# Performance work log

Measured on AMD Instinct MI355X. Metric: run time of the kernel, lower is better.

The kernel has to match this reference:

```python
import jax, jax.numpy as jnp
import numpy as np

H, W, D = 56, 56, 28            # input_resolution
WS = (7, 7, 7)                  # window size (Wh, Ww, Wd)
SS = (3, 3, 3)                  # shift size
DIM = 96
NH = 3
HD = DIM // NH
N = WS[0] * WS[1] * WS[2]       # 343 tokens per window
NW = (H // WS[0]) * (W // WS[1]) * (D // WS[2])  # 256 windows


def _rel_pos_index():
    Wd, Wh, Ww = WS
    coords = np.stack(np.meshgrid(np.arange(Wd), np.arange(Wh), np.arange(Ww), indexing='ij'))
    cf = coords.reshape(3, -1)
    rel = (cf[:, :, None] - cf[:, None, :]).transpose(1, 2, 0)
    rel[:, :, 0] += Wd - 1
    rel[:, :, 1] += Wh - 1
    rel[:, :, 2] += Ww - 1
    rel[:, :, 0] *= (2 * Wh - 1) * (2 * Ww - 1)
    rel[:, :, 1] *= (2 * Ww - 1)
    return rel.sum(-1)  # (N, N)


def _attn_mask():
    img = np.zeros((H, W, D), np.float32)
    def slices(w, s):
        return (slice(0, -w), slice(-w, -s), slice(-s, None))
    cnt = 0
    for hs in slices(WS[0], SS[0]):
        for ws in slices(WS[1], SS[1]):
            for ds in slices(WS[2], SS[2]):
                img[hs, ws, ds] = cnt
                cnt += 1
    mw = img.reshape(H // WS[0], WS[0], W // WS[1], WS[1], D // WS[2], WS[2])
    mw = mw.transpose(0, 2, 4, 1, 3, 5).reshape(-1, N)  # (NW, N)
    am = mw[:, None, :] - mw[:, :, None]
    return np.where(am != 0, np.float32(-100.0), np.float32(0.0))


REL_IDX = jnp.asarray(_rel_pos_index())
ATTN_MASK = jnp.asarray(_attn_mask())  # (NW, N, N)


def _ln(x, g, b, eps=1e-5):
    m = x.mean(-1, keepdims=True)
    v = jnp.mean((x - m) ** 2, -1, keepdims=True)
    return (x - m) * jax.lax.rsqrt(v + eps) * g + b


def _forward(x, n1g, n1b, qkv_w, qkv_b, rpb, proj_w, proj_b,
             n2g, n2b, fc1_w, fc1_b, fc2_w, fc2_b):
    B, L, C = x.shape
    shortcut = x
    h = _ln(x, n1g, n1b).reshape(B, H, W, D, C)
    # cyclic shift
    h = jnp.roll(h, (-SS[0], -SS[1], -SS[2]), axis=(1, 2, 3))
    # window partition -> (B*NW, N, C)
    h = h.reshape(B, H // WS[0], WS[0], W // WS[1], WS[1], D // WS[2], WS[2], C)
    h = h.transpose(0, 1, 3, 5, 2, 4, 6, 7).reshape(-1, N, C)
    # qkv
    qkv = (h @ qkv_w + qkv_b).reshape(-1, N, 3, NH, HD).transpose(2, 0, 3, 1, 4)
    q, k, v = qkv[0] * (HD ** -0.5), qkv[1], qkv[2]  # (B*NW, NH, N, HD)
    attn = jnp.einsum('bhnd,bhmd->bhnm', q, k)
    bias = rpb[REL_IDX.reshape(-1)].reshape(N, N, NH).transpose(2, 0, 1)
    attn = attn + bias[None]
    # shifted-window mask
    attn = attn.reshape(B, NW, NH, N, N) + ATTN_MASK[None, :, None]
    attn = jax.nn.softmax(attn.reshape(-1, NH, N, N), axis=-1)
    o = jnp.einsum('bhnm,bhmd->bhnd', attn, v).transpose(0, 2, 1, 3).reshape(-1, N, C)
    o = o @ proj_w + proj_b
    # window reverse
    o = o.reshape(B, H // WS[0], W // WS[1], D // WS[2], WS[0], WS[1], WS[2], C)
    o = o.transpose(0, 1, 4, 2, 5, 3, 6, 7).reshape(B, H, W, D, C)
    o = jnp.roll(o, SS, axis=(1, 2, 3)).reshape(B, L, C)
    x = shortcut + o
    h2 = _ln(x, n2g, n2b)
    h2 = jax.nn.gelu(h2 @ fc1_w + fc1_b, approximate=False) @ fc2_w + fc2_b
    return x + h2


def setup_inputs() -> dict:
    key = jax.random.key(0)
    ks = jax.random.split(key, 6)
    C, FF = DIM, 4 * DIM
    f32 = jnp.float32
    return {
        'x': jax.random.normal(ks[0], (1, H * W * D, C), f32),
        'n1g': jnp.ones((C,), f32), 'n1b': jnp.zeros((C,), f32),
        'qkv_w': jax.random.normal(ks[1], (C, 3 * C), f32) * 0.02,
        'qkv_b': jnp.zeros((3 * C,), f32),
        'rpb': jax.random.normal(ks[2], ((2 * WS[0] - 1) * (2 * WS[1] - 1) * (2 * WS[2] - 1), NH), f32) * 0.02,
        'proj_w': jax.random.normal(ks[3], (C, C), f32) * 0.02,
        'proj_b': jnp.zeros((C,), f32),
        'n2g': jnp.ones((C,), f32), 'n2b': jnp.zeros((C,), f32),
        'fc1_w': jax.random.normal(ks[4], (C, FF), f32) * 0.02,
        'fc1_b': jnp.zeros((FF,), f32),
        'fc2_w': jax.random.normal(ks[5], (FF, C), f32) * 0.02,
        'fc2_b': jnp.zeros((C,), f32),
    }


def reference(x, n1g, n1b, qkv_w, qkv_b, rpb, proj_w, proj_b,
              n2g, n2b, fc1_w, fc1_b, fc2_w, fc2_b):
    return _forward(x, n1g, n1b, qkv_w, qkv_b, rpb, proj_w, proj_b,
                    n2g, n2b, fc1_w, fc1_b, fc2_w, fc2_b)
```

## Files before the change

kernel.cpp:

```cpp
#include <hip/hip_runtime.h>
#include <hip/hip_bf16.h>


#define L_TOK 87808

typedef unsigned int uint;
typedef __attribute__((ext_vector_type(8))) short short8;
typedef __attribute__((ext_vector_type(4))) float f32x4;

__device__ __forceinline__ float bflo(uint u){ union{uint x; float f;} a; a.x = u << 16; return a.f; }
__device__ __forceinline__ float bfhi(uint u){ union{uint x; float f;} a; a.x = u & 0xffff0000u; return a.f; }
__device__ __forceinline__ float bfval(unsigned short w){ union{uint x; float f;} a; a.x = (uint)w << 16; return a.f; }
__device__ __forceinline__ unsigned short f2bfbits(float f){
  union{float f; uint u;} a; a.f = f;
  uint u = a.u;
  u += 0x7fffu + ((u >> 16) & 1u);
  return (unsigned short)(u >> 16);
}
__device__ __forceinline__ unsigned short bfb(float f){
  __hip_bfloat16 h = __float2bfloat16(f);
  return *reinterpret_cast<unsigned short*>(&h);
}
__device__ __forceinline__ uint pkbf(float a, float b){
  return ((uint)bfb(b) << 16) | (uint)bfb(a);
}
__device__ __forceinline__ uint pack2(float a, float b){
  return ((uint)f2bfbits(b) << 16) | (uint)f2bfbits(a);
}
__device__ __forceinline__ uint4 pack8(const float* p){
  uint4 u;
  u.x = pack2(p[0], p[1]); u.y = pack2(p[2], p[3]);
  u.z = pack2(p[4], p[5]); u.w = pack2(p[6], p[7]);
  return u;
}
__device__ __forceinline__ uint4 pack8g(const float* gp){
  float t[8];
  *(float4*)&t[0] = *(const float4*)gp;
  *(float4*)&t[4] = *(const float4*)(gp + 4);
  return pack8(t);
}
__device__ __forceinline__ float gelu_f(float v){
  const float ax = fabsf(v) * 0.70710678118654752f;
  const float t  = 1.0f / (1.0f + 0.3275911f * ax);
  const float poly = t*(0.254829592f + t*(-0.284496736f + t*(1.421413741f +
                     t*(-1.453152027f + t*1.061405429f))));
  float erfv = 1.0f - poly * __expf(-ax*ax);
  erfv = copysignf(erfv, v);
  return 0.5f * v * (1.0f + erfv);
}
__device__ __forceinline__ uint gt_of_row(uint row){
  const uint win = row / 343u, n = row % 343u;
  const uint wh = win >> 5, ww = (win >> 2) & 7u, wd = win & 3u;
  const uint ih = n / 49u, rr = n % 49u, iw = rr / 7u, id = rr % 7u;
  uint gh = wh*7u + ih + 3u; if (gh >= 56u) gh -= 56u;
  uint gw = ww*7u + iw + 3u; if (gw >= 56u) gw -= 56u;
  uint gd = wd*7u + id + 3u; if (gd >= 28u) gd -= 28u;
  return ((gh*56u + gw)*28u + gd) * 96u;
}

__global__ __launch_bounds__(256)
void k_tr(const float* __restrict__ src, unsigned short* __restrict__ dst,
          int K, int N)
{
  const int idx = blockIdx.x * 256 + threadIdx.x;
  if (idx < K * N) {
    const int n = idx / K, k = idx % K;
    dst[idx] = f2bfbits(src[(size_t)k * N + n]);
  }
}

__global__ __launch_bounds__(256)
void k_tr4(const float* __restrict__ qkvw, unsigned short* __restrict__ qkvwt,
           const float* __restrict__ pw,   unsigned short* __restrict__ pwt,
           const float* __restrict__ f1w,  unsigned short* __restrict__ w1t,
           const float* __restrict__ f2w,  unsigned short* __restrict__ w2t)
{
  const int b = blockIdx.x, tid = threadIdx.x;
  const float* src; unsigned short* dst; int K, N, idx;
  if (b < 108)      { src = qkvw; dst = qkvwt; K = 96;  N = 288; idx = b*256 + tid; }
  else if (b < 144) { src = pw;   dst = pwt;   K = 96;  N = 96;  idx = (b-108)*256 + tid; }
  else if (b < 288) { src = f1w;  dst = w1t;   K = 96;  N = 384; idx = (b-144)*256 + tid; }
  else              { src = f2w;  dst = w2t;   K = 384; N = 96;  idx = (b-288)*256 + tid; }
  if (idx < K * N) {
    const int n = idx / K, k = idx % K;
    dst[idx] = f2bfbits(src[(size_t)k * N + n]);
  }
}

__global__ __launch_bounds__(256)
void k_mb(const float* __restrict__ rpbg, unsigned short* __restrict__ MB)
{
  const int idx = blockIdx.x * 256 + threadIdx.x;
  const int cls = idx / (3*352*352);
  const int rem = idx - cls * (3*352*352);
  const int h = rem / (352*352);
  const int rem2 = rem - h * (352*352);
  const int q = rem2 / 352;
  const int k = rem2 - q * 352;
  unsigned short v = 0xFF80;
  if (q < 343 && k < 343) {
    const int q0 = q/49, q1 = (q%49)/7, q2 = q%7;
    const int k0 = k/49, k1 = (k%49)/7, k2 = k%7;
    const int bq = q0*169 + q1*13 + q2;
    const int bk = k0*169 + k1*13 + k2;
    float bias = rpbg[(size_t)(bq - bk + 1098)*3 + h];
    int cq = 0, ck = 0;
    if (cls & 4) { cq += ((q0 < 4) ? 1 : 2)*9; ck += ((k0 < 4) ? 1 : 2)*9; }
    if (cls & 2) { cq += ((q1 < 4) ? 1 : 2)*3; ck += ((k1 < 4) ? 1 : 2)*3; }
    if (cls & 1) { cq += (q2 < 4) ? 1 : 2;     ck += (k2 < 4) ? 1 : 2; }
    if (cq != ck) bias -= 100.0f;
    v = f2bfbits(bias);
  }
  MB[idx] = v;
}

__global__ __launch_bounds__(256)
void k_qkv_ln(const float* __restrict__ x,
              const float* __restrict__ n1g,
              const float* __restrict__ n1b,
              const unsigned short* __restrict__ qkvwt,
              const float* __restrict__ bias, size_t headStride,
              __hip_bfloat16* __restrict__ qb,
              __hip_bfloat16* __restrict__ kb,
              __hip_bfloat16* __restrict__ vb)
{
  __shared__ __align__(16) unsigned short As[64][104];
  __shared__ uint srcOff[64];
  __shared__ float gLds[96], bLds[96];
  __shared__ float pSum[256], pSq[256];
  __shared__ float mLds[64], sLds[64];

  const int tid = threadIdx.x;
  const int wave = tid >> 6, lane = tid & 63;
  const int row0 = blockIdx.x * 64;

  if (tid < 64) srcOff[tid] = gt_of_row((uint)(row0 + tid));
  if (tid < 96) { gLds[tid] = n1g[tid]; bLds[tid] = n1b[tid]; }
  __syncthreads();

  for (int i = tid; i < 768; i += 256) {
    const int r = i / 12, kk = (i % 12) * 8;
    *(uint4*)&As[r][kk] = pack8g(x + srcOff[r] + kk);
  }
  __syncthreads();

  {
    const int r = tid & 63, seg = tid >> 6;
    float s = 0.0f, sq = 0.0f;
    #pragma unroll
    for (int j3 = 0; j3 < 3; ++j3) {
      const uint4 u = *(const uint4*)&As[r][seg*24 + j3*8];
      float v[8];
      v[0]=bflo(u.x); v[1]=bfhi(u.x); v[2]=bflo(u.y); v[3]=bfhi(u.y);
      v[4]=bflo(u.z); v[5]=bfhi(u.z); v[6]=bflo(u.w); v[7]=bfhi(u.w);
      #pragma unroll
      for (int j = 0; j < 8; ++j) { s += v[j]; sq += v[j]*v[j]; }
    }
    pSum[tid] = s; pSq[tid] = sq;
  }
  __syncthreads();
  if (tid < 64) {
    const float s  = pSum[tid] + pSum[tid+64] + pSum[tid+128] + pSum[tid+192];
    const float sq = pSq[tid] + pSq[tid+64] + pSq[tid+128] + pSq[tid+192];
    const float mean = s * (1.0f/96.0f);
    mLds[tid] = mean;
    sLds[tid] = rsqrtf(sq*(1.0f/96.0f) - mean*mean + 1e-5f);
  }
  __syncthreads();
  for (int i = tid; i < 768; i += 256) {
    const int r = i / 12, kk = (i % 12) * 8;
    uint4 u = *(uint4*)&As[r][kk];
    const float m = mLds[r], sc = sLds[r];
    float v[8];
    v[0]=bflo(u.x); v[1]=bfhi(u.x); v[2]=bflo(u.y); v[3]=bfhi(u.y);
    v[4]=bflo(u.z); v[5]=bfhi(u.z); v[6]=bflo(u.w); v[7]=bfhi(u.w);
    #pragma unroll
    for (int j = 0; j < 8; ++j) v[j] = (v[j] - m)*sc*gLds[kk+j] + bLds[kk+j];
    *(uint4*)&As[r][kk] = pack8(v);
  }
  __syncthreads();

  f32x4 acc[18];
  #pragma unroll
  for (int i = 0; i < 18; ++i) acc[i] = (f32x4){0.f, 0.f, 0.f, 0.f};
  const int ml = lane & 15, q8 = (lane >> 4) * 8;
  #pragma unroll
  for (int kc = 0; kc < 3; ++kc) {
    const short8 a = *(const short8*)&As[wave*16 + ml][kc*32 + q8];
    #pragma unroll
    for (int nt = 0; nt < 18; ++nt) {
      const short8 b = *(const short8*)(qkvwt + (size_t)(nt*16 + ml)*96 + kc*32 + q8);
      acc[nt] = __builtin_amdgcn_mfma_f32_16x16x32_bf16(a, b, acc[nt], 0, 0, 0);
    }
  }

  const float qscale = 0.17677669529663687f;
  #pragma unroll
  for (int nt = 0; nt < 18; ++nt) {
    const int nbase = nt * 16;
    const int part = nbase / 96;
    const int rem  = nbase - part * 96;
    const int h    = rem >> 5;
    const int dbase= rem & 31;
    __hip_bfloat16* base = (part == 0) ? qb : ((part == 1) ? kb : vb);
    __hip_bfloat16* dst = base + (size_t)h * headStride;
    const float bv = bias[nbase + ml];
    #pragma unroll
    for (int r = 0; r < 4; ++r) {
      const size_t row = (size_t)(row0 + wave*16 + (lane >> 4)*4 + r);
      float v = acc[nt][r] + bv;
      if (part == 0) v *= qscale;
      dst[row*32 + dbase + ml] = __float2bfloat16(v);
    }
  }
}

template<bool BF16OUT>
__global__ __launch_bounds__(256, 4)
void k_attn_v10(const __hip_bfloat16* __restrict__ qg,
                const __hip_bfloat16* __restrict__ kg,
                const __hip_bfloat16* __restrict__ vg,
                size_t headStride,
                const unsigned short* __restrict__ MB,
                void* __restrict__ obp)
{
  __shared__ __align__(16) unsigned short vt[32*344 + 16];
  __shared__ __align__(16) unsigned short Pc[4][16*56];
  __shared__ float lred[4][16];

  const int tid = threadIdx.x;
  const int wave = tid >> 6, lane = tid & 63;
  const uint win = blockIdx.x;
  const int hh = (int)blockIdx.y;
  const int mtBase = (int)blockIdx.z * 11;
  const size_t wbase = (size_t)hh * headStride + (size_t)win * (343*32);
  const unsigned short* qw = (const unsigned short*)qg + wbase;
  const unsigned short* kw = (const unsigned short*)kg + wbase;
  const unsigned short* vw = (const unsigned short*)vg + wbase;

  const uint wh = win >> 5, ww = (win >> 2) & 7u, wd = win & 3u;
  const int cls = ((wh == 7u) ? 4 : 0) | ((ww == 7u) ? 2 : 0) | ((wd == 3u) ? 1 : 0);
  const unsigned short* MBh = MB + ((size_t)cls*3 + hh) * (352*352);

  for (int t = tid; t < 343; t += 256) {
    const uint4* src = (const uint4*)(vw + (size_t)t*32);
    #pragma unroll
    for (int c4 = 0; c4 < 4; ++c4) {
      const uint4 u = src[c4];
      const int d = c4*8;
      vt[(d+0)*344 + t] = (unsigned short)(u.x & 0xffffu);
      vt[(d+1)*344 + t] = (unsigned short)(u.x >> 16);
      vt[(d+2)*344 + t] = (unsigned short)(u.y & 0xffffu);
      vt[(d+3)*344 + t] = (unsigned short)(u.y >> 16);
      vt[(d+4)*344 + t] = (unsigned short)(u.z & 0xffffu);
      vt[(d+5)*344 + t] = (unsigned short)(u.z >> 16);
      vt[(d+6)*344 + t] = (unsigned short)(u.w & 0xffffu);
      vt[(d+7)*344 + t] = (unsigned short)(u.w >> 16);
    }
  }
  if (tid < 32) vt[tid*344 + 343] = 0;
  if (tid < 16) vt[32*344 + tid] = 0;
  __syncthreads();

  const int ml = lane & 15, g = lane >> 4, g8 = g*8;
  unsigned short* Pw = &Pc[wave][0];

  for (int mt = mtBase + wave; mt < mtBase + 11; mt += 4) {
    const int q = mt*16 + ml;
    const short8 qf = *(const short8*)(qw + (size_t)q*32 + g8);
    const unsigned short* MBq = MBh + (size_t)q * 352;
    float l = 0.0f;
    f32x4 o0 = {0.f,0.f,0.f,0.f}, o1 = {0.f,0.f,0.f,0.f};

    for (int kc = 0; kc < 11; ++kc) {
      const short8 kf0 = *(const short8*)(kw + (size_t)(kc*32 + ml)*32 + g8);
      const short8 kf1 = *(const short8*)(kw + (size_t)(kc*32 + 16 + ml)*32 + g8);
      f32x4 s0 = __builtin_amdgcn_mfma_f32_16x16x32_bf16(kf0, qf, (f32x4){0.f,0.f,0.f,0.f}, 0, 0, 0);
      f32x4 s1 = __builtin_amdgcn_mfma_f32_16x16x32_bf16(kf1, qf, (f32x4){0.f,0.f,0.f,0.f}, 0, 0, 0);

      const ushort4 u0 = *(const ushort4*)(MBq + kc*32 + 4*g);
      const ushort4 u1 = *(const ushort4*)(MBq + kc*32 + 16 + 4*g);

      float p0 = __expf(s0[0] + bfval(u0.x));
      float p1 = __expf(s0[1] + bfval(u0.y));
      float p2 = __expf(s0[2] + bfval(u0.z));
      float p3 = __expf(s0[3] + bfval(u0.w));
      float p4 = __expf(s1[0] + bfval(u1.x));
      float p5 = __expf(s1[1] + bfval(u1.y));
      float p6 = __expf(s1[2] + bfval(u1.z));
      float p7 = __expf(s1[3] + bfval(u1.w));
      l += ((p0 + p1) + (p2 + p3)) + ((p4 + p5) + (p6 + p7));

      uint2 wlo, whi;
      wlo.x = pkbf(p0, p1); wlo.y = pkbf(p2, p3);
      whi.x = pkbf(p4, p5); whi.y = pkbf(p6, p7);
      *(uint2*)&Pw[ml*56 + 4*g]      = wlo;
      *(uint2*)&Pw[ml*56 + 16 + 4*g] = whi;

      const short8 pf  = *(const short8*)&Pw[ml*56 + g8];
      const short8 vf0 = *(const short8*)&vt[(size_t)ml*344 + kc*32 + g8];
      const short8 vf1 = *(const short8*)&vt[(size_t)(16 + ml)*344 + kc*32 + g8];
      o0 = __builtin_amdgcn_mfma_f32_16x16x32_bf16(pf, vf0, o0, 0, 0, 0);
      o1 = __builtin_amdgcn_mfma_f32_16x16x32_bf16(pf, vf1, o1, 0, 0, 0);
    }

    l += __shfl_xor(l, 16);
    l += __shfl_xor(l, 32);
    if (g == 0) lred[wave][ml] = 1.0f / l;
    const float4 li = *(const float4*)&lred[wave][4*g];
    #pragma unroll
    for (int r = 0; r < 4; ++r) {
      const int row = mt*16 + 4*g + r;
      if (row < 343) {
        const size_t base = ((size_t)win*343 + (uint)row)*96 + hh*32;
        if (BF16OUT) {
          __hip_bfloat16* op = (__hip_bfloat16*)obp + base;
          op[ml]      = __float2bfloat16(o0[r] * li[r]);
          op[16 + ml] = __float2bfloat16(o1[r] * li[r]);
        } else {
          float* op = (float*)obp + base;
          op[ml]      = o0[r] * li[r];
          op[16 + ml] = o1[r] * li[r];
        }
      }
    }
  }
}

__global__ __launch_bounds__(256, 3)
void k_pm(const __hip_bfloat16* __restrict__ obb,
          const unsigned short* __restrict__ pwt,
          const float* __restrict__ pb,
          const float* __restrict__ xin,
          const float* __restrict__ n2g,
          const float* __restrict__ n2b,
          const unsigned short* __restrict__ w1t,
          const float* __restrict__ b1,
          const unsigned short* __restrict__ w2t,
          const float* __restrict__ b2,
          float* __restrict__ out)
{
  __shared__ __align__(16) unsigned short As[64][104];
  __shared__ __align__(16) unsigned short Rs[64][104];
  __shared__ __align__(16) unsigned short inter[64][200];
  __shared__ uint gtO[64];

  const int tid = threadIdx.x;
  const int wave = tid >> 6, lane = tid & 63;
  const int row0 = blockIdx.x * 64;
  const int ml = lane & 15, g = lane >> 4, g8 = g*8;

  uint gtr[4];
  #pragma unroll
  for (int r = 0; r < 4; ++r) gtr[r] = gt_of_row((uint)(row0 + wave*16 + 4*g + r));
  float xv[4][6];
  #pragma unroll
  for (int r = 0; r < 4; ++r)
    #pragma unroll
    for (int nt = 0; nt < 6; ++nt)
      xv[r][nt] = xin[(size_t)gtr[r] + nt*16 + ml];
  float pbv[6], gv[6], bvv[6];
  #pragma unroll
  for (int nt = 0; nt < 6; ++nt) {
    pbv[nt] = pb[nt*16 + ml];
    gv[nt]  = n2g[nt*16 + ml];
    bvv[nt] = n2b[nt*16 + ml];
  }
  float b1a[3], b1b[3], b2v[3];
  const int cbp = 48 * (wave & 1);
  #pragma unroll
  for (int nt = 0; nt < 3; ++nt) {
    b1a[nt] = b1[48*wave + 16*nt + ml];
    b1b[nt] = b1[192 + 48*wave + 16*nt + ml];
    b2v[nt] = b2[cbp + 16*nt + ml];
  }
  if (tid < 64) gtO[tid] = gt_of_row((uint)(row0 + tid));
  for (int i = tid; i < 768; i += 256) {
    const int r = i / 12, kk = (i % 12) * 8;
    *(uint4*)&As[r][kk] = *(const uint4*)(obb + (size_t)(row0 + r)*96 + kk);
  }
  __syncthreads();

  f32x4 acc[6];
  #pragma unroll
  for (int i = 0; i < 6; ++i) acc[i] = (f32x4){0.f, 0.f, 0.f, 0.f};
  #pragma unroll
  for (int kc = 0; kc < 3; ++kc) {
    const short8 a = *(const short8*)&As[wave*16 + ml][kc*32 + g8];
    #pragma unroll
    for (int nt = 0; nt < 6; ++nt) {
      const short8 b = *(const short8*)(pwt + (size_t)(nt*16 + ml)*96 + kc*32 + g8);
      acc[nt] = __builtin_amdgcn_mfma_f32_16x16x32_bf16(a, b, acc[nt], 0, 0, 0);
    }
  }

  short8 bf[3][3];
  #pragma unroll
  for (int nt = 0; nt < 3; ++nt)
    #pragma unroll
    for (int kc = 0; kc < 3; ++kc)
      bf[nt][kc] = *(const short8*)(w1t + (size_t)(48*wave + 16*nt + ml)*96 + kc*32 + g8);

  float vr[4][6];
  float s[4] = {0.f,0.f,0.f,0.f}, sq[4] = {0.f,0.f,0.f,0.f};
  #pragma unroll
  for (int r = 0; r < 4; ++r) {
    const int row = wave*16 + 4*g + r;
    #pragma unroll
    for (int nt = 0; nt < 6; ++nt) {
      const float v = acc[nt][r] + pbv[nt] + xv[r][nt];
      const unsigned short ub = f2bfbits(v);
      Rs[row][nt*16 + ml] = ub;
      const float vv = bfval(ub);
      vr[r][nt] = vv;
      s[r] += vv; sq[r] += vv*vv;
    }
  }
  #pragma unroll
  for (int r = 0; r < 4; ++r) {
    #pragma unroll
    for (int m = 1; m <= 8; m <<= 1) {
      s[r]  += __shfl_xor(s[r],  m);
      sq[r] += __shfl_xor(sq[r], m);
    }
    const float mean = s[r] * (1.0f/96.0f);
    const float rstd = rsqrtf(sq[r]*(1.0f/96.0f) - mean*mean + 1e-5f);
    const int row = wave*16 + 4*g + r;
    #pragma unroll
    for (int nt = 0; nt < 6; ++nt)
      As[row][nt*16 + ml] = f2bfbits((vr[r][nt] - mean)*rstd*gv[nt] + bvv[nt]);
  }
  __syncthreads();

  short8 af[4][3];
  #pragma unroll
  for (int mt = 0; mt < 4; ++mt)
    #pragma unroll
    for (int kc = 0; kc < 3; ++kc)
      af[mt][kc] = *(const short8*)&As[mt*16 + ml][kc*32 + g8];

  const int rb = 32 * (wave >> 1);
  const int cb = cbp;
  f32x4 acc2[2][3];
  #pragma unroll
  for (int i = 0; i < 2; ++i)
    #pragma unroll
    for (int nt = 0; nt < 3; ++nt)
      acc2[i][nt] = (f32x4){0.f, 0.f, 0.f, 0.f};

  short8 bf1[3][3];

  {
    f32x4 a1[4][3];
    #pragma unroll
    for (int mt = 0; mt < 4; ++mt)
      #pragma unroll
      for (int nt = 0; nt < 3; ++nt)
        a1[mt][nt] = (f32x4){0.f, 0.f, 0.f, 0.f};
    #pragma unroll
    for (int kc = 0; kc < 3; ++kc)
      #pragma unroll
      for (int nt = 0; nt < 3; ++nt)
        #pragma unroll
        for (int mt = 0; mt < 4; ++mt)
          a1[mt][nt] = __builtin_amdgcn_mfma_f32_16x16x32_bf16(af[mt][kc], bf[nt][kc], a1[mt][nt], 0, 0, 0);

    #pragma unroll
    for (int nt = 0; nt < 3; ++nt)
      #pragma unroll
      for (int kc = 0; kc < 3; ++kc)
        bf1[nt][kc] = *(const short8*)(w1t + (size_t)(192 + 48*wave + 16*nt + ml)*96 + kc*32 + g8);

    #pragma unroll
    for (int nt = 0; nt < 3; ++nt) {
      const int c = 48*wave + 16*nt + ml;
      #pragma unroll
      for (int mt = 0; mt < 4; ++mt)
        #pragma unroll
        for (int r = 0; r < 4; ++r)
          inter[mt*16 + 4*g + r][c] = f2bfbits(gelu_f(a1[mt][nt][r] + b1a[nt]));
    }
  }
  __syncthreads();

  #pragma unroll
  for (int kcl = 0; kcl < 6; ++kcl) {
    const short8 a0 = *(const short8*)&inter[rb + ml][kcl*32 + g8];
    const short8 a1 = *(const short8*)&inter[rb + 16 + ml][kcl*32 + g8];
    #pragma unroll
    for (int nt = 0; nt < 3; ++nt) {
      const short8 b = *(const short8*)(w2t + (size_t)(cb + 16*nt + ml)*384 + kcl*32 + g8);
      acc2[0][nt] = __builtin_amdgcn_mfma_f32_16x16x32_bf16(a0, b, acc2[0][nt], 0, 0, 0);
      acc2[1][nt] = __builtin_amdgcn_mfma_f32_16x16x32_bf16(a1, b, acc2[1][nt], 0, 0, 0);
    }
  }
  __syncthreads();

  {
    f32x4 a1[4][3];
    #pragma unroll
    for (int mt = 0; mt < 4; ++mt)
      #pragma unroll
      for (int nt = 0; nt < 3; ++nt)
        a1[mt][nt] = (f32x4){0.f, 0.f, 0.f, 0.f};
    #pragma unroll
    for (int kc = 0; kc < 3; ++kc)
      #pragma unroll
      for (int nt = 0; nt < 3; ++nt)
        #pragma unroll
        for (int mt = 0; mt < 4; ++mt)
          a1[mt][nt] = __builtin_amdgcn_mfma_f32_16x16x32_bf16(af[mt][kc], bf1[nt][kc], a1[mt][nt], 0, 0, 0);

    #pragma unroll
    for (int nt = 0; nt < 3; ++nt) {
      const int c = 48*wave + 16*nt + ml;
      #pragma unroll
      for (int mt = 0; mt < 4; ++mt)
        #pragma unroll
        for (int r = 0; r < 4; ++r)
          inter[mt*16 + 4*g + r][c] = f2bfbits(gelu_f(a1[mt][nt][r] + b1b[nt]));
    }
  }
  __syncthreads();

  #pragma unroll
  for (int kcl = 0; kcl < 6; ++kcl) {
    const short8 a0 = *(const short8*)&inter[rb + ml][kcl*32 + g8];
    const short8 a1 = *(const short8*)&inter[rb + 16 + ml][kcl*32 + g8];
    #pragma unroll
    for (int nt = 0; nt < 3; ++nt) {
      const short8 b = *(const short8*)(w2t + (size_t)(cb + 16*nt + ml)*384 + 192 + kcl*32 + g8);
      acc2[0][nt] = __builtin_amdgcn_mfma_f32_16x16x32_bf16(a0, b, acc2[0][nt], 0, 0, 0);
      acc2[1][nt] = __builtin_amdgcn_mfma_f32_16x16x32_bf16(a1, b, acc2[1][nt], 0, 0, 0);
    }
  }

  #pragma unroll
  for (int i = 0; i < 2; ++i) {
    #pragma unroll
    for (int nt = 0; nt < 3; ++nt) {
      const int col = cb + 16*nt + ml;
      #pragma unroll
      for (int r = 0; r < 4; ++r) {
        const int rl = rb + 16*i + 4*g + r;
        out[(size_t)gtO[rl] + col] = acc2[i][nt][r] + b2v[nt] + bfval(Rs[rl][col]);
      }
    }
  }
}

__global__ __launch_bounds__(256)
void k_proj(const float* __restrict__ A,
            const unsigned short* __restrict__ pwt,
            const float* __restrict__ bias,
            const float* __restrict__ xin,
            __hip_bfloat16* __restrict__ xres)
{
  __shared__ __align__(16) unsigned short As[128][104];
  const int tid = threadIdx.x;
  const int wave = tid >> 6, lane = tid & 63;
  const int row0 = blockIdx.x * 128;

  for (int i = tid; i < 1536; i += 256) {
    const int r = i / 12, kk = (i % 12) * 8;
    *(uint4*)&As[r][kk] = pack8g(A + (size_t)(row0 + r)*96 + kk);
  }
  __syncthreads();

  f32x4 acc[2][6];
  #pragma unroll
  for (int mt = 0; mt < 2; ++mt)
    #pragma unroll
    for (int i = 0; i < 6; ++i) acc[mt][i] = (f32x4){0.f, 0.f, 0.f, 0.f};
  const int ml = lane & 15, q8 = (lane >> 4) * 8;
  #pragma unroll
  for (int kc = 0; kc < 3; ++kc) {
    const short8 a0 = *(const short8*)&As[wave*32 + ml][kc*32 + q8];
    const short8 a1 = *(const short8*)&As[wave*32 + 16 + ml][kc*32 + q8];
    #pragma unroll
    for (int nt = 0; nt < 6; ++nt) {
      const short8 b = *(const short8*)(pwt + (size_t)(nt*16 + ml)*96 + kc*32 + q8);
      acc[0][nt] = __builtin_amdgcn_mfma_f32_16x16x32_bf16(a0, b, acc[0][nt], 0, 0, 0);
      acc[1][nt] = __builtin_amdgcn_mfma_f32_16x16x32_bf16(a1, b, acc[1][nt], 0, 0, 0);
    }
  }

  #pragma unroll
  for (int mt = 0; mt < 2; ++mt) {
    #pragma unroll
    for (int r = 0; r < 4; ++r) {
      const uint row = (uint)(row0 + wave*32 + mt*16 + (lane >> 4)*4 + r);
      const size_t gt = (size_t)gt_of_row(row);
      #pragma unroll
      for (int nt = 0; nt < 6; ++nt) {
        const int col = nt*16 + ml;
        xres[gt + col] = __float2bfloat16(acc[mt][nt][r] + bias[col] + xin[gt + col]);
      }
    }
  }
}

__global__ __launch_bounds__(256, 4)
void k_mlp(const __hip_bfloat16* __restrict__ xresb,
           const float* __restrict__ n2g,
           const float* __restrict__ n2b,
           const unsigned short* __restrict__ w1t,
           const float* __restrict__ b1,
           const unsigned short* __restrict__ w2t,
           const float* __restrict__ b2,
           float* __restrict__ out)
{
  __shared__ __align__(16) unsigned short As[64][104];
  __shared__ __align__(16) unsigned short inter[64][200];
  float* scr  = (float*)&inter[0][0];
  float* pSum = scr;
  float* pSq  = scr + 256;
  float* gL   = scr + 512;
  float* bL   = scr + 608;
  float* mL   = scr + 704;
  float* sL   = scr + 768;

  const int tid = threadIdx.x;
  const int wave = tid >> 6, lane = tid & 63;
  const int row0 = blockIdx.x * 64;
  const int ml = lane & 15, g = lane >> 4, g8 = g*8;

  if (tid < 96) { gL[tid] = n2g[tid]; bL[tid] = n2b[tid]; }
  for (int i = tid; i < 768; i += 256) {
    const int r = i / 12, kk = (i % 12) * 8;
    *(uint4*)&As[r][kk] = *(const uint4*)(xresb + (size_t)(row0 + r)*96 + kk);
  }
  __syncthreads();

  {
    const int r = tid & 63, seg = tid >> 6;
    float s = 0.0f, sq = 0.0f;
    #pragma unroll
    for (int j3 = 0; j3 < 3; ++j3) {
      const uint4 u = *(const uint4*)&As[r][seg*24 + j3*8];
      float v[8];
      v[0]=bflo(u.x); v[1]=bfhi(u.x); v[2]=bflo(u.y); v[3]=bfhi(u.y);
      v[4]=bflo(u.z); v[5]=bfhi(u.z); v[6]=bflo(u.w); v[7]=bfhi(u.w);
      #pragma unroll
      for (int j = 0; j < 8; ++j) { s += v[j]; sq += v[j]*v[j]; }
    }
    pSum[tid] = s; pSq[tid] = sq;
  }
  __syncthreads();
  if (tid < 64) {
    const float s  = pSum[tid] + pSum[tid+64] + pSum[tid+128] + pSum[tid+192];
    const float sq = pSq[tid] + pSq[tid+64] + pSq[tid+128] + pSq[tid+192];
    const float mean = s * (1.0f/96.0f);
    mL[tid] = mean;
    sL[tid] = rsqrtf(sq*(1.0f/96.0f) - mean*mean + 1e-5f);
  }
  __syncthreads();
  for (int i = tid; i < 768; i += 256) {
    const int r = i / 12, kk = (i % 12) * 8;
    uint4 u = *(uint4*)&As[r][kk];
    const float m = mL[r], sc = sL[r];
    float v[8];
    v[0]=bflo(u.x); v[1]=bfhi(u.x); v[2]=bflo(u.y); v[3]=bfhi(u.y);
    v[4]=bflo(u.z); v[5]=bfhi(u.z); v[6]=bflo(u.w); v[7]=bfhi(u.w);
    #pragma unroll
    for (int j = 0; j < 8; ++j) v[j] = (v[j] - m)*sc*gL[kk+j] + bL[kk+j];
    *(uint4*)&As[r][kk] = pack8(v);
  }
  __syncthreads();

  short8 af[4][3];
  #pragma unroll
  for (int mt = 0; mt < 4; ++mt)
    #pragma unroll
    for (int kc = 0; kc < 3; ++kc)
      af[mt][kc] = *(const short8*)&As[mt*16 + ml][kc*32 + g8];

  const int rb = 32 * (wave >> 1);
  const int cb = 48 * (wave & 1);
  f32x4 acc2[2][3];
  #pragma unroll
  for (int i = 0; i < 2; ++i)
    #pragma unroll
    for (int nt = 0; nt < 3; ++nt)
      acc2[i][nt] = (f32x4){0.f, 0.f, 0.f, 0.f};

  #pragma unroll
  for (int H = 0; H < 2; ++H) {
    if (H) __syncthreads();

    const int nbg = H*192 + 48*wave;
    const int cl0 = 48*wave;
    short8 bf[3][3];
    #pragma unroll
    for (int nt = 0; nt < 3; ++nt)
      #pragma unroll
      for (int kc = 0; kc < 3; ++kc)
        bf[nt][kc] = *(const short8*)(w1t + (size_t)(nbg + 16*nt + ml)*96 + kc*32 + g8);

    f32x4 acc[4][3];
    #pragma unroll
    for (int mt = 0; mt < 4; ++mt)
      #pragma unroll
      for (int nt = 0; nt < 3; ++nt)
        acc[mt][nt] = (f32x4){0.f, 0.f, 0.f, 0.f};

    #pragma unroll
    for (int kc = 0; kc < 3; ++kc)
      #pragma unroll
      for (int nt = 0; nt < 3; ++nt)
        #pragma unroll
        for (int mt = 0; mt < 4; ++mt)
          acc[mt][nt] = __builtin_amdgcn_mfma_f32_16x16x32_bf16(af[mt][kc], bf[nt][kc], acc[mt][nt], 0, 0, 0);

    #pragma unroll
    for (int nt = 0; nt < 3; ++nt) {
      const float b1v = b1[nbg + 16*nt + ml];
      const int c = cl0 + 16*nt + ml;
      #pragma unroll
      for (int mt = 0; mt < 4; ++mt) {
        #pragma unroll
        for (int r = 0; r < 4; ++r) {
          inter[mt*16 + 4*g + r][c] = f2bfbits(gelu_f(acc[mt][nt][r] + b1v));
        }
      }
    }
    __syncthreads();

    #pragma unroll
    for (int kcl = 0; kcl < 6; ++kcl) {
      const short8 a0 = *(const short8*)&inter[rb + ml][kcl*32 + g8];
      const short8 a1 = *(const short8*)&inter[rb + 16 + ml][kcl*32 + g8];
      #pragma unroll
      for (int nt = 0; nt < 3; ++nt) {
        const short8 b = *(const short8*)(w2t + (size_t)(cb + 16*nt + ml)*384 + H*192 + kcl*32 + g8);
        acc2[0][nt] = __builtin_amdgcn_mfma_f32_16x16x32_bf16(a0, b, acc2[0][nt], 0, 0, 0);
        acc2[1][nt] = __builtin_amdgcn_mfma_f32_16x16x32_bf16(a1, b, acc2[1][nt], 0, 0, 0);
      }
    }
  }

  const unsigned short* xu = (const unsigned short*)xresb;
  #pragma unroll
  for (int i = 0; i < 2; ++i) {
    #pragma unroll
    for (int nt = 0; nt < 3; ++nt) {
      const int col = cb + 16*nt + ml;
      const float b2v = b2[col];
      #pragma unroll
      for (int r = 0; r < 4; ++r) {
        const size_t row = (size_t)(row0 + rb + 16*i + 4*g + r);
        out[row*96 + col] = acc2[i][nt][r] + b2v + bfval(xu[row*96 + col]);
      }
    }
  }
}

extern "C" void kernel_launch(void* const* d_in, const int* in_sizes, int n_in,
                              void* d_out, int out_size, void* d_ws, size_t ws_size,
                              hipStream_t stream)
{
  (void)in_sizes; (void)n_in; (void)out_size;
  const float* x    = (const float*)d_in[0];
  const float* n1g  = (const float*)d_in[1];
  const float* n1b  = (const float*)d_in[2];
  const float* qkvw = (const float*)d_in[3];
  const float* qkvb = (const float*)d_in[4];
  const float* rpb  = (const float*)d_in[5];
  const float* pw   = (const float*)d_in[6];
  const float* pb   = (const float*)d_in[7];
  const float* n2g  = (const float*)d_in[8];
  const float* n2b  = (const float*)d_in[9];
  const float* f1w  = (const float*)d_in[10];
  const float* f1b  = (const float*)d_in[11];
  const float* f2w  = (const float*)d_in[12];
  const float* f2b  = (const float*)d_in[13];
  float* out = (float*)d_out;

  const size_t E = (size_t)L_TOK * 96;
  __hip_bfloat16* qb = (__hip_bfloat16*)d_ws;
  __hip_bfloat16* kb = qb + E;
  __hip_bfloat16* vb = kb + E;
  __hip_bfloat16* xres = (__hip_bfloat16*)d_ws;
  const size_t hs = (size_t)L_TOK * 32;

  unsigned short* qkvwt = (unsigned short*)d_out;

  const size_t MB_BYTES = (size_t)8 * 3 * 352 * 352 * 2;
  const size_t WT_BYTES = (size_t)(9216 + 36864 + 36864) * 2;
  const size_t off_mb  = (size_t)6 * E;
  const size_t off_obb = off_mb + MB_BYTES;
  const size_t off_wt  = off_obb + (size_t)2 * E;
  const bool mbok  = ws_size >= off_obb;
  const bool fused = ws_size >= off_wt;
  const bool tier1 = ws_size >= off_wt + WT_BYTES;

  unsigned short* MBp = mbok ? (unsigned short*)((char*)d_ws + off_mb) : nullptr;
  __hip_bfloat16* obb = fused ? (__hip_bfloat16*)((char*)d_ws + off_obb) : nullptr;

  if (MBp) k_mb<<<11616, 256, 0, stream>>>(rpb, MBp);

  if (tier1) {
    unsigned short* pwt = (unsigned short*)((char*)d_ws + off_wt);
    unsigned short* w1t = pwt + 9216;
    unsigned short* w2t = w1t + 36864;
    k_tr4<<<432, 256, 0, stream>>>(qkvw, qkvwt, pw, pwt, f1w, w1t, f2w, w2t);
    k_qkv_ln<<<L_TOK/64, 256, 0, stream>>>(x, n1g, n1b, qkvwt, qkvb, hs, qb, kb, vb);
    k_attn_v10<true><<<dim3(256, 3, 2), 256, 0, stream>>>(qb, kb, vb, hs, MBp, (void*)obb);
    k_pm<<<L_TOK/64, 256, 0, stream>>>(obb, pwt, pb, x, n2g, n2b,
                                       w1t, f1b, w2t, f2b, out);
  } else {
    unsigned short* pwt = (unsigned short*)kb;
    unsigned short* w1t = pwt + 9216;
    unsigned short* w2t = w1t + 36864;
    k_tr<<<108, 256, 0, stream>>>(qkvw, qkvwt, 96, 288);
    k_qkv_ln<<<L_TOK/64, 256, 0, stream>>>(x, n1g, n1b, qkvwt, qkvb, hs, qb, kb, vb);
    if (fused) {
      k_attn_v10<true><<<dim3(256, 3, 2), 256, 0, stream>>>(qb, kb, vb, hs, MBp, (void*)obb);
      k_tr<<<36, 256, 0, stream>>>(pw, pwt, 96, 96);
      k_tr<<<144, 256, 0, stream>>>(f1w, w1t, 96, 384);
      k_tr<<<144, 256, 0, stream>>>(f2w, w2t, 384, 96);
      k_pm<<<L_TOK/64, 256, 0, stream>>>(obb, pwt, pb, x, n2g, n2b,
                                         w1t, f1b, w2t, f2b, out);
    } else {
      float* ob = out;
      k_attn_v10<false><<<dim3(256, 3, 2), 256, 0, stream>>>(qb, kb, vb, hs, MBp, (void*)ob);
      k_tr<<<36, 256, 0, stream>>>(pw, pwt, 96, 96);
      k_tr<<<144, 256, 0, stream>>>(f1w, w1t, 96, 384);
      k_tr<<<144, 256, 0, stream>>>(f2w, w2t, 384, 96);
      k_proj<<<L_TOK/128, 256, 0, stream>>>(ob, pwt, pb, x, xres);
      k_mlp<<<L_TOK/64, 256, 0, stream>>>(xres, n2g, n2b, w1t, f1b, w2t, f2b, out);
    }
  }
}
```

Measured before the change: 272.3 us.

## Compute LayerNorm in registers and feed MFMA fragments directly in qkv kernel

```diff
diff --git a/kernel.cpp b/kernel.cpp
--- a/kernel.cpp
+++ b/kernel.cpp
@@ -114,7 +114,7 @@
   MB[idx] = v;
 }
 
-__global__ __launch_bounds__(256)
+__global__ __launch_bounds__(256, 3)
 void k_qkv_ln(const float* __restrict__ x,
               const float* __restrict__ n1g,
               const float* __restrict__ n1b,
@@ -124,73 +124,56 @@
               __hip_bfloat16* __restrict__ kb,
               __hip_bfloat16* __restrict__ vb)
 {
-  __shared__ __align__(16) unsigned short As[64][104];
-  __shared__ uint srcOff[64];
-  __shared__ float gLds[96], bLds[96];
-  __shared__ float pSum[256], pSq[256];
-  __shared__ float mLds[64], sLds[64];
-
   const int tid = threadIdx.x;
   const int wave = tid >> 6, lane = tid & 63;
+  const int ml = lane & 15, g = lane >> 4, g8 = g*8;
   const int row0 = blockIdx.x * 64;
-
-  if (tid < 64) srcOff[tid] = gt_of_row((uint)(row0 + tid));
-  if (tid < 96) { gLds[tid] = n1g[tid]; bLds[tid] = n1b[tid]; }
-  __syncthreads();
-
-  for (int i = tid; i < 768; i += 256) {
-    const int r = i / 12, kk = (i % 12) * 8;
-    *(uint4*)&As[r][kk] = pack8g(x + srcOff[r] + kk);
-  }
-  __syncthreads();
-
-  {
-    const int r = tid & 63, seg = tid >> 6;
-    float s = 0.0f, sq = 0.0f;
-    #pragma unroll
-    for (int j3 = 0; j3 < 3; ++j3) {
-      const uint4 u = *(const uint4*)&As[r][seg*24 + j3*8];
-      float v[8];
-      v[0]=bflo(u.x); v[1]=bfhi(u.x); v[2]=bflo(u.y); v[3]=bfhi(u.y);
-      v[4]=bflo(u.z); v[5]=bfhi(u.z); v[6]=bflo(u.w); v[7]=bfhi(u.w);
-      #pragma unroll
-      for (int j = 0; j < 8; ++j) { s += v[j]; sq += v[j]*v[j]; }
-    }
-    pSum[tid] = s; pSq[tid] = sq;
-  }
-  __syncthreads();
-  if (tid < 64) {
-    const float s  = pSum[tid] + pSum[tid+64] + pSum[tid+128] + pSum[tid+192];
-    const float sq = pSq[tid] + pSq[tid+64] + pSq[tid+128] + pSq[tid+192];
-    const float mean = s * (1.0f/96.0f);
-    mLds[tid] = mean;
-    sLds[tid] = rsqrtf(sq*(1.0f/96.0f) - mean*mean + 1e-5f);
-  }
-  __syncthreads();
-  for (int i = tid; i < 768; i += 256) {
-    const int r = i / 12, kk = (i % 12) * 8;
-    uint4 u = *(uint4*)&As[r][kk];
-    const float m = mLds[r], sc = sLds[r];
-    float v[8];
-    v[0]=bflo(u.x); v[1]=bfhi(u.x); v[2]=bflo(u.y); v[3]=bfhi(u.y);
-    v[4]=bflo(u.z); v[5]=bfhi(u.z); v[6]=bflo(u.w); v[7]=bfhi(u.w);
-    #pragma unroll
-    for (int j = 0; j < 8; ++j) v[j] = (v[j] - m)*sc*gLds[kk+j] + bLds[kk+j];
-    *(uint4*)&As[r][kk] = pack8(v);
-  }
-  __syncthreads();
+  const uint myrow = (uint)(row0 + wave*16 + ml);
+  const uint src = gt_of_row(myrow);
+
+  float vv[24];
+  float s = 0.f, sq = 0.f;
+  #pragma unroll
+  for (int kc = 0; kc < 3; ++kc) {
+    float t[8];
+    *(float4*)&t[0] = *(const float4*)(x + src + kc*32 + g8);
+    *(float4*)&t[4] = *(const float4*)(x + src + kc*32 + g8 + 4);
+    #pragma unroll
+    for (int j = 0; j < 8; ++j) {
+      const float v = bfval(f2bfbits(t[j]));
+      vv[kc*8 + j] = v;
+      s += v; sq += v*v;
+    }
+  }
+  s  += __shfl_xor(s, 16);  s  += __shfl_xor(s, 32);
+  sq += __shfl_xor(sq, 16); sq += __shfl_xor(sq, 32);
+  const float mean = s * (1.0f/96.0f);
+  const float rstd = rsqrtf(sq*(1.0f/96.0f) - mean*mean + 1e-5f);
+
+  short8 afrag[3];
+  #pragma unroll
+  for (int kc = 0; kc < 3; ++kc) {
+    float gm[8], bt[8], v[8];
+    *(float4*)&gm[0] = *(const float4*)(n1g + kc*32 + g8);
+    *(float4*)&gm[4] = *(const float4*)(n1g + kc*32 + g8 + 4);
+    *(float4*)&bt[0] = *(const float4*)(n1b + kc*32 + g8);
+    *(float4*)&bt[4] = *(const float4*)(n1b + kc*32 + g8 + 4);
+    #pragma unroll
+    for (int j = 0; j < 8; ++j)
+      v[j] = (vv[kc*8 + j] - mean)*rstd*gm[j] + bt[j];
+    uint4 u = pack8(v);
+    afrag[kc] = *(short8*)&u;
+  }
 
   f32x4 acc[18];
   #pragma unroll
   for (int i = 0; i < 18; ++i) acc[i] = (f32x4){0.f, 0.f, 0.f, 0.f};
-  const int ml = lane & 15, q8 = (lane >> 4) * 8;
   #pragma unroll
   for (int kc = 0; kc < 3; ++kc) {
-    const short8 a = *(const short8*)&As[wave*16 + ml][kc*32 + q8];
     #pragma unroll
     for (int nt = 0; nt < 18; ++nt) {
-      const short8 b = *(const short8*)(qkvwt + (size_t)(nt*16 + ml)*96 + kc*32 + q8);
-      acc[nt] = __builtin_amdgcn_mfma_f32_16x16x32_bf16(a, b, acc[nt], 0, 0, 0);
+      const short8 b = *(const short8*)(qkvwt + (size_t)(nt*16 + ml)*96 + kc*32 + g8);
+      acc[nt] = __builtin_amdgcn_mfma_f32_16x16x32_bf16(afrag[kc], b, acc[nt], 0, 0, 0);
     }
   }
 
@@ -207,7 +190,7 @@
     const float bv = bias[nbase + ml];
     #pragma unroll
     for (int r = 0; r < 4; ++r) {
-      const size_t row = (size_t)(row0 + wave*16 + (lane >> 4)*4 + r);
+      const size_t row = (size_t)(row0 + wave*16 + 4*g + r);
       float v = acc[nt][r] + bv;
       if (part == 0) v *= qscale;
       dst[row*32 + dbase + ml] = __float2bfloat16(v);
```

After: 267.3 us. No clear change (-1.8%).
